# Performance work log

Hardware: AMD Instinct MI355X
Metric: run time of the kernel (lower is better)

## Reference

```python
import jax, jax.numpy as jnp
import numpy as np

RNN = 1024
ATT_HID = 512
ATT_FEAT = 2048
ENC = 1024  # input_encoding_size == rnn_size
B = 256
ATT_SIZE = 196


def setup_inputs() -> dict:
    key = jax.random.key(0)
    ks = jax.random.split(key, 9)
    s = lambda fan_in: 1.0 / np.sqrt(fan_in)
    return {
        "h": jax.random.normal(ks[0], (B, RNN), jnp.float32),
        "att_feats": jax.random.normal(ks[1], (B, ATT_SIZE, ATT_FEAT), jnp.float32),
        "p_att_feats": jax.random.normal(ks[2], (B, ATT_SIZE, 2 * ATT_HID), jnp.float32),
        # h2att: Linear(rnn_size, 2*att_hid_size)
        "W_h2att": jax.random.uniform(ks[3], (RNN, 2 * ATT_HID), jnp.float32, -s(RNN), s(RNN)),
        "b_h2att": jax.random.uniform(ks[4], (2 * ATT_HID,), jnp.float32, -s(RNN), s(RNN)),
        # alpha_net: Linear(att_hid_size, 1)
        "w_alpha": jax.random.uniform(ks[5], (ATT_HID,), jnp.float32, -s(ATT_HID), s(ATT_HID)),
        "b_alpha": jax.random.uniform(ks[6], (), jnp.float32, -s(ATT_HID), s(ATT_HID)),
        # att_out: Linear(att_feat_size, 2*input_encoding_size)
        "W_out": jax.random.uniform(ks[7], (ATT_FEAT, 2 * ENC), jnp.float32, -s(ATT_FEAT), s(ATT_FEAT)),
        "b_out": jax.random.uniform(ks[8], (2 * ENC,), jnp.float32, -s(ATT_FEAT), s(ATT_FEAT)),
    }


def reference(h, att_feats, p_att_feats, W_h2att, b_h2att, w_alpha, b_alpha, W_out, b_out):
    # att_h: [B, 2*ATT_HID], broadcast-added over att_size
    att_h = h @ W_h2att + b_h2att
    dot = p_att_feats + att_h[:, None, :]                      # [B, S, 2*H]
    gated = jnp.tanh(dot[..., :ATT_HID]) * jax.nn.sigmoid(dot[..., ATT_HID:])  # [B, S, H]
    scores = jnp.einsum("bsh,h->bs", gated, w_alpha) + b_alpha  # [B, S]
    weight = jax.nn.softmax(scores, axis=-1)                    # [B, S]
    att_res = jnp.einsum("bs,bsf->bf", weight, att_feats)       # [B, ATT_FEAT]
    out = att_res @ W_out + b_out                               # [B, 2*ENC]
    return jnp.tanh(out[:, :RNN]) * jax.nn.sigmoid(out[:, RNN:2 * RNN])  # [B, RNN]
```

## Files before the change

kernel.cpp:

```cpp
#include <hip/hip_runtime.h>

using bf16x8 = __attribute__((ext_vector_type(8))) short;
using f32x4  = __attribute__((ext_vector_type(4))) float;

__device__ __forceinline__ ushort f2bf(float f) {
    union { float f; uint i; } v; v.f = f;
    uint r = v.i + 0x7fffu + ((v.i >> 16) & 1u);
    return (ushort)(r >> 16);
}
__device__ __forceinline__ float gate1(float x1, float x2) {
    float e1 = __expf(2.f * x1);
    float e2 = __expf(-x2);
    return (e1 - 1.f) * __builtin_amdgcn_rcpf((e1 + 1.f) * (1.f + e2));
}

__global__ __launch_bounds__(256) void k_cvt(const float* __restrict__ src,
                                             ushort* __restrict__ dst) {
    int i = (blockIdx.x * 256 + threadIdx.x) * 4;
    float4 v = *(const float4*)(src + i);
    uint2 o;
    o.x = (uint)f2bf(v.x) | ((uint)f2bf(v.y) << 16);
    o.y = (uint)f2bf(v.z) | ((uint)f2bf(v.w) << 16);
    *(uint2*)(dst + i) = o;
}

__global__ __launch_bounds__(256) void k_cvt_transpose(const float* __restrict__ src,
                                                       ushort* __restrict__ dst,
                                                       int R, int C) {
    __shared__ float t[32][33];
    int c0 = blockIdx.x << 5, r0 = blockIdx.y << 5;
    int x = threadIdx.x & 31, y = threadIdx.x >> 5;
#pragma unroll
    for (int j = 0; j < 4; j++)
        t[y + 8 * j][x] = src[(size_t)(r0 + y + 8 * j) * C + c0 + x];
    __syncthreads();
#pragma unroll
    for (int j = 0; j < 4; j++)
        dst[(size_t)(c0 + y + 8 * j) * R + r0 + x] = f2bf(t[x][y + 8 * j]);
}

__global__ __launch_bounds__(256) void k_gemm_bt(const ushort* __restrict__ A,
                                                 const ushort* __restrict__ BT,
                                                 float* __restrict__ Cp,
                                                 int M, int N, int K, int kchunk) {
    __shared__ ushort As[64 * 40];
    __shared__ ushort Bs[64 * 40];
    const int tid = threadIdx.x;
    const int n0 = blockIdx.x << 6, m0 = blockIdx.y << 6;
    const int k0 = blockIdx.z * kchunk;
    const int wave = tid >> 6, lane = tid & 63;
    const int wm = (wave >> 1) << 5, wn = (wave & 1) << 5;
    const int lr = lane & 15, lq = lane >> 4;
    const int srow = tid >> 2, scol = (tid & 3) << 3;

    f32x4 acc00 = {0.f, 0.f, 0.f, 0.f}, acc01 = acc00, acc10 = acc00, acc11 = acc00;
    const ushort* Ap = A + (size_t)(m0 + srow) * K + k0 + scol;
    const ushort* Bp = BT + (size_t)(n0 + srow) * K + k0 + scol;
    ushort* asd = &As[srow * 40 + scol];
    ushort* bsd = &Bs[srow * 40 + scol];

    for (int k = 0; k < kchunk; k += 32) {
        *(uint4*)asd = *(const uint4*)(Ap + k);
        *(uint4*)bsd = *(const uint4*)(Bp + k);
        __syncthreads();
        bf16x8 a0 = *(const bf16x8*)&As[(wm + lr) * 40 + (lq << 3)];
        bf16x8 a1 = *(const bf16x8*)&As[(wm + 16 + lr) * 40 + (lq << 3)];
        bf16x8 b0 = *(const bf16x8*)&Bs[(wn + lr) * 40 + (lq << 3)];
        bf16x8 b1 = *(const bf16x8*)&Bs[(wn + 16 + lr) * 40 + (lq << 3)];
        acc00 = __builtin_amdgcn_mfma_f32_16x16x32_bf16(a0, b0, acc00, 0, 0, 0);
        acc01 = __builtin_amdgcn_mfma_f32_16x16x32_bf16(a0, b1, acc01, 0, 0, 0);
        acc10 = __builtin_amdgcn_mfma_f32_16x16x32_bf16(a1, b0, acc10, 0, 0, 0);
        acc11 = __builtin_amdgcn_mfma_f32_16x16x32_bf16(a1, b1, acc11, 0, 0, 0);
        __syncthreads();
    }
    float* Cb = Cp + (size_t)blockIdx.z * M * N + (size_t)(m0 + wm + lq * 4) * N + n0 + wn + lr;
#pragma unroll
    for (int r = 0; r < 4; r++) {
        Cb[(size_t)r * N]             = acc00[r];
        Cb[(size_t)r * N + 16]        = acc01[r];
        Cb[(size_t)(r + 16) * N]      = acc10[r];
        Cb[(size_t)(r + 16) * N + 16] = acc11[r];
    }
}

__global__ __launch_bounds__(256) void k_reduce_bias(const float* __restrict__ part,
                                                     const float* __restrict__ bias,
                                                     float* __restrict__ outp,
                                                     int MN, int Nmask) {
    int idx = blockIdx.x * 256 + threadIdx.x;
    float s = bias[idx & Nmask];
#pragma unroll
    for (int ks = 0; ks < 4; ks++) s += part[ks * MN + idx];
    outp[idx] = s;
}

__global__ __launch_bounds__(256) void k_scores(const float* __restrict__ p,
                                                const float* __restrict__ att_h,
                                                const float* __restrict__ w_alpha,
                                                const float* __restrict__ b_alpha,
                                                float* __restrict__ scores) {
    int wid = (blockIdx.x << 2) + (threadIdx.x >> 6);
    int lane = threadIdx.x & 63;
    int b = wid / 196;
    const float* pr = p + (size_t)wid * 1024 + lane * 8;
    float4 p1a = *(const float4*)pr;
    float4 p1b = *(const float4*)(pr + 4);
    float4 p2a = *(const float4*)(pr + 512);
    float4 p2b = *(const float4*)(pr + 516);
    const float* ah = att_h + ((size_t)b << 10) + lane * 8;
    float4 a1a = *(const float4*)ah;
    float4 a1b = *(const float4*)(ah + 4);
    float4 a2a = *(const float4*)(ah + 512);
    float4 a2b = *(const float4*)(ah + 516);
    const float* wa = w_alpha + lane * 8;
    float4 w0 = *(const float4*)wa;
    float4 w1 = *(const float4*)(wa + 4);
    float sum = gate1(p1a.x + a1a.x, p2a.x + a2a.x) * w0.x
              + gate1(p1a.y + a1a.y, p2a.y + a2a.y) * w0.y
              + gate1(p1a.z + a1a.z, p2a.z + a2a.z) * w0.z
              + gate1(p1a.w + a1a.w, p2a.w + a2a.w) * w0.w
              + gate1(p1b.x + a1b.x, p2b.x + a2b.x) * w1.x
              + gate1(p1b.y + a1b.y, p2b.y + a2b.y) * w1.y
              + gate1(p1b.z + a1b.z, p2b.z + a2b.z) * w1.z
              + gate1(p1b.w + a1b.w, p2b.w + a2b.w) * w1.w;
#pragma unroll
    for (int off = 32; off; off >>= 1) sum += __shfl_down(sum, off);
    if (lane == 0) scores[wid] = sum + b_alpha[0];
}

__global__ __launch_bounds__(256) void k_softmax(const float* __restrict__ scores,
                                                 float* __restrict__ wts) {
    int b = blockIdx.x, t = threadIdx.x;
    __shared__ float red[16];
    float v = (t < 196) ? scores[b * 196 + t] : -3.4e38f;
    float m = v;
#pragma unroll
    for (int off = 32; off; off >>= 1) m = fmaxf(m, __shfl_down(m, off));
    int wv = t >> 6, ln = t & 63;
    if (ln == 0) red[wv] = m;
    __syncthreads();
    if (t == 0) red[8] = fmaxf(fmaxf(red[0], red[1]), fmaxf(red[2], red[3]));
    __syncthreads();
    float M = red[8];
    float e = (t < 196) ? __expf(v - M) : 0.f;
    float s = e;
#pragma unroll
    for (int off = 32; off; off >>= 1) s += __shfl_down(s, off);
    if (ln == 0) red[wv + 4] = s;
    __syncthreads();
    if (t == 0) red[9] = 1.f / (red[4] + red[5] + red[6] + red[7]);
    __syncthreads();
    if (t < 196) wts[b * 196 + t] = e * red[9];
}

__global__ __launch_bounds__(256) void k_attres(const float* __restrict__ feats,
                                                const float* __restrict__ wts,
                                                ushort* __restrict__ att_res) {
    int b = blockIdx.x >> 1, fh = blockIdx.x & 1;
    __shared__ float wl[196];
    if (threadIdx.x < 196) wl[threadIdx.x] = wts[b * 196 + threadIdx.x];
    __syncthreads();
    int f = (fh << 10) + threadIdx.x * 4;
    const float* base = feats + (size_t)b * 196 * 2048 + f;
    float a0 = 0.f, a1 = 0.f, a2 = 0.f, a3 = 0.f;
    for (int s = 0; s < 196; s += 7) {
        float4 q0 = *(const float4*)(base + (size_t)(s + 0) * 2048);
        float4 q1 = *(const float4*)(base + (size_t)(s + 1) * 2048);
        float4 q2 = *(const float4*)(base + (size_t)(s + 2) * 2048);
        float4 q3 = *(const float4*)(base + (size_t)(s + 3) * 2048);
        float4 q4 = *(const float4*)(base + (size_t)(s + 4) * 2048);
        float4 q5 = *(const float4*)(base + (size_t)(s + 5) * 2048);
        float4 q6 = *(const float4*)(base + (size_t)(s + 6) * 2048);
        float w0 = wl[s + 0], w1 = wl[s + 1], w2 = wl[s + 2], w3 = wl[s + 3];
        float w4 = wl[s + 4], w5 = wl[s + 5], w6 = wl[s + 6];
        a0 += w0 * q0.x + w1 * q1.x + w2 * q2.x + w3 * q3.x + w4 * q4.x + w5 * q5.x + w6 * q6.x;
        a1 += w0 * q0.y + w1 * q1.y + w2 * q2.y + w3 * q3.y + w4 * q4.y + w5 * q5.y + w6 * q6.y;
        a2 += w0 * q0.z + w1 * q1.z + w2 * q2.z + w3 * q3.z + w4 * q4.z + w5 * q5.z + w6 * q6.z;
        a3 += w0 * q0.w + w1 * q1.w + w2 * q2.w + w3 * q3.w + w4 * q4.w + w5 * q5.w + w6 * q6.w;
    }
    uint2 o;
    o.x = (uint)f2bf(a0) | ((uint)f2bf(a1) << 16);
    o.y = (uint)f2bf(a2) | ((uint)f2bf(a3) << 16);
    *(uint2*)(att_res + ((size_t)b << 11) + f) = o;
}

__global__ __launch_bounds__(256) void k_gate_out(const float* __restrict__ part,
                                                  const float* __restrict__ b_out,
                                                  float* __restrict__ outp) {
    int idx = blockIdx.x * 256 + threadIdx.x;
    int b = idx >> 10, i = idx & 1023;
    int c1 = (b << 11) + i;
    const int MN = 256 * 2048;
    float o1 = b_out[i];
    float o2 = b_out[i + 1024];
#pragma unroll
    for (int ks = 0; ks < 2; ks++) {
        o1 += part[ks * MN + c1];
        o2 += part[ks * MN + c1 + 1024];
    }
    outp[idx] = gate1(o1, o2);
}

extern "C" void kernel_launch(void* const* d_in, const int* in_sizes, int n_in,
                              void* d_out, int out_size, void* d_ws, size_t ws_size,
                              hipStream_t stream) {
    const float* h         = (const float*)d_in[0];
    const float* att_feats = (const float*)d_in[1];
    const float* p_att     = (const float*)d_in[2];
    const float* W_h2att   = (const float*)d_in[3];
    const float* b_h2att   = (const float*)d_in[4];
    const float* w_alpha   = (const float*)d_in[5];
    const float* b_alpha   = (const float*)d_in[6];
    const float* W_out     = (const float*)d_in[7];
    const float* b_out     = (const float*)d_in[8];
    float* outp = (float*)d_out;

    char* w = (char*)d_ws;
    const size_t KB = 1024;
    ushort* hbf     = (ushort*)w;
    ushort* WT1     = (ushort*)(w + 512 * KB);
    ushort* WT2     = (ushort*)(w + 2560 * KB);
    float*  part1   = (float*)(w + 10752 * KB);
    float*  part5   = (float*)(w + 10752 * KB);
    float*  att_h   = (float*)(w + 14848 * KB);
    float*  scores  = (float*)(w + 15872 * KB);
    ushort* att_res = (ushort*)(w + 16128 * KB);

    k_cvt<<<256, 256, 0, stream>>>(h, hbf);
    k_cvt_transpose<<<dim3(32, 32), 256, 0, stream>>>(W_h2att, WT1, 1024, 1024);
    k_cvt_transpose<<<dim3(64, 64), 256, 0, stream>>>(W_out, WT2, 2048, 2048);
    k_gemm_bt<<<dim3(16, 4, 4), 256, 0, stream>>>(hbf, WT1, part1, 256, 1024, 1024, 256);
    k_reduce_bias<<<1024, 256, 0, stream>>>(part1, b_h2att, att_h, 256 * 1024, 1023);
    k_scores<<<12544, 256, 0, stream>>>(p_att, att_h, w_alpha, b_alpha, scores);
    k_softmax<<<256, 256, 0, stream>>>(scores, scores);
    k_attres<<<512, 256, 0, stream>>>(att_feats, scores, att_res);
    k_gemm_bt<<<dim3(32, 4, 2), 256, 0, stream>>>(att_res, WT2, part5, 256, 2048, 2048, 1024);
    k_gate_out<<<1024, 256, 0, stream>>>(part5, b_out, outp);
}
```

Baseline: 697.1 us.

## Fuse prep conversions into one kernel and softmax into attention-weighted sum

Merges the h conversion and both weight transpose-conversions into a single launch, with block-index ranges selecting the task. Folds the softmax into the attention-weighted reduction kernel, so each block recomputes its batch row's softmax in shared memory instead of a separate launch writing weights to global memory. Deepens the att_feats load batch from 7 to 14 float4 loads per iteration to raise memory-level parallelism. This cuts launches and a small round trip, at the cost of higher register pressure and duplicated softmax work across the two feature halves.

```diff
diff --git a/kernel.cpp b/kernel.cpp
--- a/kernel.cpp
+++ b/kernel.cpp
@@ -14,21 +14,11 @@
     return (e1 - 1.f) * __builtin_amdgcn_rcpf((e1 + 1.f) * (1.f + e2));
 }
 
-__global__ __launch_bounds__(256) void k_cvt(const float* __restrict__ src,
-                                             ushort* __restrict__ dst) {
-    int i = (blockIdx.x * 256 + threadIdx.x) * 4;
-    float4 v = *(const float4*)(src + i);
-    uint2 o;
-    o.x = (uint)f2bf(v.x) | ((uint)f2bf(v.y) << 16);
-    o.y = (uint)f2bf(v.z) | ((uint)f2bf(v.w) << 16);
-    *(uint2*)(dst + i) = o;
-}
-
-__global__ __launch_bounds__(256) void k_cvt_transpose(const float* __restrict__ src,
-                                                       ushort* __restrict__ dst,
-                                                       int R, int C) {
-    __shared__ float t[32][33];
-    int c0 = blockIdx.x << 5, r0 = blockIdx.y << 5;
+__device__ __forceinline__ void transpose_tile(const float* __restrict__ src,
+                                               ushort* __restrict__ dst,
+                                               int R, int C, int bx, int by,
+                                               float (*t)[33]) {
+    int c0 = bx << 5, r0 = by << 5;
     int x = threadIdx.x & 31, y = threadIdx.x >> 5;
 #pragma unroll
     for (int j = 0; j < 4; j++)
@@ -37,6 +27,30 @@
 #pragma unroll
     for (int j = 0; j < 4; j++)
         dst[(size_t)(c0 + y + 8 * j) * R + r0 + x] = f2bf(t[x][y + 8 * j]);
+}
+
+__global__ __launch_bounds__(256) void k_prep(const float* __restrict__ h,
+                                              ushort* __restrict__ hbf,
+                                              const float* __restrict__ W1,
+                                              ushort* __restrict__ WT1,
+                                              const float* __restrict__ W2,
+                                              ushort* __restrict__ WT2) {
+    __shared__ float t[32][33];
+    int bid = blockIdx.x;
+    if (bid < 4096) {
+        transpose_tile(W2, WT2, 2048, 2048, bid & 63, bid >> 6, t);
+    } else if (bid < 4096 + 1024) {
+        int r = bid - 4096;
+        transpose_tile(W1, WT1, 1024, 1024, r & 31, r >> 5, t);
+    } else {
+        int r = bid - 5120;
+        int i = (r * 256 + threadIdx.x) * 4;
+        float4 v = *(const float4*)(h + i);
+        uint2 o;
+        o.x = (uint)f2bf(v.x) | ((uint)f2bf(v.y) << 16);
+        o.y = (uint)f2bf(v.z) | ((uint)f2bf(v.w) << 16);
+        *(uint2*)(hbf + i) = o;
+    }
 }
 
 __global__ __launch_bounds__(256) void k_gemm_bt(const ushort* __restrict__ A,
@@ -128,10 +142,13 @@
     if (lane == 0) scores[wid] = sum + b_alpha[0];
 }
 
-__global__ __launch_bounds__(256) void k_softmax(const float* __restrict__ scores,
-                                                 float* __restrict__ wts) {
-    int b = blockIdx.x, t = threadIdx.x;
+__global__ __launch_bounds__(256) void k_attres_sm(const float* __restrict__ feats,
+                                                   const float* __restrict__ scores,
+                                                   ushort* __restrict__ att_res) {
+    int b = blockIdx.x >> 1, fh = blockIdx.x & 1;
+    __shared__ float wl[196];
     __shared__ float red[16];
+    int t = threadIdx.x;
     float v = (t < 196) ? scores[b * 196 + t] : -3.4e38f;
     float m = v;
 #pragma unroll
@@ -150,33 +167,25 @@
     __syncthreads();
     if (t == 0) red[9] = 1.f / (red[4] + red[5] + red[6] + red[7]);
     __syncthreads();
-    if (t < 196) wts[b * 196 + t] = e * red[9];
-}
-
-__global__ __launch_bounds__(256) void k_attres(const float* __restrict__ feats,
-                                                const float* __restrict__ wts,
-                                                ushort* __restrict__ att_res) {
-    int b = blockIdx.x >> 1, fh = blockIdx.x & 1;
-    __shared__ float wl[196];
-    if (threadIdx.x < 196) wl[threadIdx.x] = wts[b * 196 + threadIdx.x];
-    __syncthreads();
-    int f = (fh << 10) + threadIdx.x * 4;
+    if (t < 196) wl[t] = e * red[9];
+    __syncthreads();
+    int f = (fh << 10) + t * 4;
     const float* base = feats + (size_t)b * 196 * 2048 + f;
     float a0 = 0.f, a1 = 0.f, a2 = 0.f, a3 = 0.f;
-    for (int s = 0; s < 196; s += 7) {
-        float4 q0 = *(const float4*)(base + (size_t)(s + 0) * 2048);
-        float4 q1 = *(const float4*)(base + (size_t)(s + 1) * 2048);
-        float4 q2 = *(const float4*)(base + (size_t)(s + 2) * 2048);
-        float4 q3 = *(const float4*)(base + (size_t)(s + 3) * 2048);
-        float4 q4 = *(const float4*)(base + (size_t)(s + 4) * 2048);
-        float4 q5 = *(const float4*)(base + (size_t)(s + 5) * 2048);
-        float4 q6 = *(const float4*)(base + (size_t)(s + 6) * 2048);
-        float w0 = wl[s + 0], w1 = wl[s + 1], w2 = wl[s + 2], w3 = wl[s + 3];
-        float w4 = wl[s + 4], w5 = wl[s + 5], w6 = wl[s + 6];
-        a0 += w0 * q0.x + w1 * q1.x + w2 * q2.x + w3 * q3.x + w4 * q4.x + w5 * q5.x + w6 * q6.x;
-        a1 += w0 * q0.y + w1 * q1.y + w2 * q2.y + w3 * q3.y + w4 * q4.y + w5 * q5.y + w6 * q6.y;
-        a2 += w0 * q0.z + w1 * q1.z + w2 * q2.z + w3 * q3.z + w4 * q4.z + w5 * q5.z + w6 * q6.z;
-        a3 += w0 * q0.w + w1 * q1.w + w2 * q2.w + w3 * q3.w + w4 * q4.w + w5 * q5.w + w6 * q6.w;
+    for (int s0 = 0; s0 < 196; s0 += 14) {
+        float4 q[14];
+        float w[14];
+#pragma unroll
+        for (int j = 0; j < 14; j++) q[j] = *(const float4*)(base + (size_t)(s0 + j) * 2048);
+#pragma unroll
+        for (int j = 0; j < 14; j++) w[j] = wl[s0 + j];
+#pragma unroll
+        for (int j = 0; j < 14; j++) {
+            a0 += w[j] * q[j].x;
+            a1 += w[j] * q[j].y;
+            a2 += w[j] * q[j].z;
+            a3 += w[j] * q[j].w;
+        }
     }
     uint2 o;
     o.x = (uint)f2bf(a0) | ((uint)f2bf(a1) << 16);
@@ -226,14 +235,11 @@
     float*  scores  = (float*)(w + 15872 * KB);
     ushort* att_res = (ushort*)(w + 16128 * KB);
 
-    k_cvt<<<256, 256, 0, stream>>>(h, hbf);
-    k_cvt_transpose<<<dim3(32, 32), 256, 0, stream>>>(W_h2att, WT1, 1024, 1024);
-    k_cvt_transpose<<<dim3(64, 64), 256, 0, stream>>>(W_out, WT2, 2048, 2048);
+    k_prep<<<5376, 256, 0, stream>>>(h, hbf, W_h2att, WT1, W_out, WT2);
     k_gemm_bt<<<dim3(16, 4, 4), 256, 0, stream>>>(hbf, WT1, part1, 256, 1024, 1024, 256);
     k_reduce_bias<<<1024, 256, 0, stream>>>(part1, b_h2att, att_h, 256 * 1024, 1023);
     k_scores<<<12544, 256, 0, stream>>>(p_att, att_h, w_alpha, b_alpha, scores);
-    k_softmax<<<256, 256, 0, stream>>>(scores, scores);
-    k_attres<<<512, 256, 0, stream>>>(att_feats, scores, att_res);
+    k_attres_sm<<<512, 256, 0, stream>>>(att_feats, scores, att_res);
     k_gemm_bt<<<dim3(32, 4, 2), 256, 0, stream>>>(att_res, WT2, part5, 256, 2048, 2048, 1024);
     k_gate_out<<<1024, 256, 0, stream>>>(part5, b_out, outp);
 }
```

Result: no change. 691.6 us (-0.8%).
